# Optimization experiments

Hardware: AMD Instinct MI355X
Metric: run time of the kernel (lower is better)

Reference implementation:

```python
import jax, jax.numpy as jnp
import numpy as np
from jax import lax

N_QUBITS = 4
N_LAYERS = 1
K = 4       # kernel_size = n_qubits
S = 2       # stride
CDTYPE = jnp.complex64


def _rz(theta):
    # theta: (B,) or scalar -> (B,2,2) or (2,2) complex RZ matrix diag(e^{-i t/2}, e^{i t/2})
    p = jnp.exp(-0.5j * theta.astype(CDTYPE))
    q = jnp.exp(0.5j * theta.astype(CDTYPE))
    z = jnp.zeros_like(p)
    return jnp.stack([jnp.stack([p, z], -1), jnp.stack([z, q], -1)], -2)


def _ry(theta):
    c = jnp.cos(theta / 2).astype(CDTYPE)
    s = jnp.sin(theta / 2).astype(CDTYPE)
    return jnp.stack([jnp.stack([c, -s], -1), jnp.stack([s, c], -1)], -2)


def _apply_1q(state, U, wire):
    # state: (B,2,2,2,2); U: (B,2,2) per-sample or (2,2) shared
    s = jnp.moveaxis(state, 1 + wire, -1)
    if U.ndim == 3:
        s = jnp.einsum('bij,b...j->b...i', U, s)
    else:
        s = jnp.einsum('ij,b...j->b...i', U, s)
    return jnp.moveaxis(s, -1, 1 + wire)


def _apply_crz(state, theta, c, t):
    # CRZ is diagonal: diag(1,1,e^{-i t/2},e^{+i t/2}) in |control,target> basis
    one = jnp.ones((), CDTYPE)
    d = jnp.stack([jnp.stack([one, one]),
                   jnp.stack([jnp.exp(-0.5j * theta).astype(CDTYPE),
                              jnp.exp(0.5j * theta).astype(CDTYPE)])])  # (2,2)[ctrl,tgt]
    s = jnp.moveaxis(state, [1 + c, 1 + t], [-2, -1])
    return jnp.moveaxis(s * d, [-2, -1], [1 + c, 1 + t])


def _qcircuit(inputs, weights):
    # inputs: (B, 16) encoding angles; weights: (n_layers, 2*n_qubits)
    B, n_in = inputs.shape
    var_per_qubit = n_in // N_QUBITS + 1  # = 5 for 16 inputs
    # Hadamard on every qubit applied to |0000> gives the uniform state (amp = 1/4)
    state = jnp.full((B,) + (2,) * N_QUBITS, 0.25, dtype=CDTYPE)
    # data encoding: alternating RZ/RY per qubit
    for q in range(N_QUBITS):
        for i in range(var_per_qubit):
            idx = q * var_per_qubit + i
            if idx < n_in:
                theta = inputs[:, idx]
                U = _rz(theta) if i % 2 == 0 else _ry(theta)
                state = _apply_1q(state, U, q)
    # variational layer(s): ring of CRZ then RY on each wire
    for l in range(weights.shape[0]):
        for i in range(N_QUBITS):
            state = _apply_crz(state, weights[l, i], i, (i + 1) % N_QUBITS)
        for j in range(N_QUBITS):
            state = _apply_1q(state, _ry(weights[l, N_QUBITS + j]), j)
    # <Z_q> expectation values
    p = (state * jnp.conj(state)).real  # (B,2,2,2,2)
    evs = []
    for q in range(N_QUBITS):
        axes = tuple(a for a in range(1, 1 + N_QUBITS) if a != 1 + q)
        pq = jnp.sum(p, axis=axes)  # (B,2)
        evs.append(pq[:, 0] - pq[:, 1])
    return jnp.stack(evs, -1)  # (B, 4)


def reference(X, weights):
    # X: (B, 1, H, W)
    B = X.shape[0]
    # all sliding 4x4/stride-2 patches, feature order (c, kh, kw) matches torch.flatten
    patches = lax.conv_general_dilated_patches(X, (K, K), (S, S), 'VALID')  # (B,16,ox,oy)
    ox, oy = patches.shape[2], patches.shape[3]
    flat = jnp.transpose(patches, (0, 2, 3, 1)).reshape(B * ox * oy, -1)  # row-major patch order
    out = _qcircuit(flat, weights)  # (B*ox*oy, 4)
    # reproduce torch.cat(dim=1).view(bs, n_qubits, ox, oy) ordering exactly
    return out.reshape(B, ox * oy * N_QUBITS).reshape(B, N_QUBITS, ox, oy)


def setup_inputs() -> dict:
    key = jax.random.key(0)
    kx, kw = jax.random.split(key)
    X = jax.random.normal(kx, (128, 1, 192, 192), dtype=jnp.float32)
    weights = jax.random.normal(kw, (N_LAYERS, 2 * N_QUBITS), dtype=jnp.float32)
    return {"X": X, "weights": weights}
```

## Files before the change

### kernel.cpp

```cpp
#include <hip/hip_runtime.h>

namespace {

constexpr int IMG = 192;
constexpr int OX = 95, OY = 95;
constexpr int NPB = OX * OY;
constexpr int BATCH = 128;
constexpr int JP = 48;
constexpr int PERIMG = OX * JP;
constexpr int TOTAL = BATCH * PERIMG;
constexpr int NWG = TOTAL / 256;
constexpr int CHUNK = NWG / 8;

__device__ __forceinline__ float2 cmul(float2 a, float2 b) {
    return make_float2(a.x*b.x - a.y*b.y, a.x*b.y + a.y*b.x);
}

__device__ __forceinline__ void qubit_chain(
    float s0, float c0, float s1, float c1, float s2, float c2,
    float s3, float c3, float s4, float c4,
    float& m, float2& cq)
{
    float C0 = c0*c0 - s0*s0, S0 = 2.f*s0*c0;
    float C2 = c2*c2 - s2*s2, S2 = 2.f*s2*c2;
    float C4 = c4*c4 - s4*s4, S4f = 2.f*s4*c4;
    float2 u0 = make_float2(c1 - s1*C0, -s1*S0);
    float2 u1 = make_float2(s1 + c1*C0,  c1*S0);
    u1 = cmul(u1, make_float2(C2, S2));
    float2 n0 = make_float2(c3*u0.x - s3*u1.x, c3*u0.y - s3*u1.y);
    float2 n1 = make_float2(s3*u0.x + c3*u1.x, s3*u0.y + c3*u1.y);
    n1 = cmul(n1, make_float2(C4, S4f));
    m  = (n0.x*n0.x + n0.y*n0.y) - (n1.x*n1.x + n1.y*n1.y);
    cq = make_float2(n0.x*n1.x + n0.y*n1.y, n0.x*n1.y - n0.y*n1.x);
}

__device__ __forceinline__ float4 patch_ev(
    const float sh[4][6], const float ch[4][6], int o,
    const float cw[4], const float sw[4], const float ehx[4], const float ehy[4],
    const float Kq[4], const float S4v[4])
{
    float m[4]; float2 cq[4];
    qubit_chain(sh[0][o+0],ch[0][o+0], sh[0][o+1],ch[0][o+1], sh[0][o+2],ch[0][o+2],
                sh[0][o+3],ch[0][o+3], sh[1][o+0],ch[1][o+0], m[0], cq[0]);
    qubit_chain(sh[1][o+1],ch[1][o+1], sh[1][o+2],ch[1][o+2], sh[1][o+3],ch[1][o+3],
                sh[2][o+0],ch[2][o+0], sh[2][o+1],ch[2][o+1], m[1], cq[1]);
    qubit_chain(sh[2][o+2],ch[2][o+2], sh[2][o+3],ch[2][o+3], sh[3][o+0],ch[3][o+0],
                sh[3][o+1],ch[3][o+1], sh[3][o+2],ch[3][o+2], m[2], cq[2]);
    {
        float s = sh[3][o+3], c = ch[3][o+3];
        m[3]  = 0.f;
        cq[3] = make_float2(c*c - s*s, 2.f*s*c);
    }

    float ev[4];
#pragma unroll
    for (int q = 0; q < 4; ++q) {
        int jm = (q + 3) & 3, jp = (q + 1) & 3;
        float hmC = 0.5f * m[jm];
        float2 aC = make_float2((1.f + cw[jm]) + hmC * (1.f - cw[jm]),
                                sw[jm] * (1.f - hmC));
        float hmT = 0.5f * m[jp];
        float2 aT = make_float2((1.f + cw[q]) + hmT * (1.f - cw[q]),
                                sw[q] * (1.f - hmT));
        float2 t = cmul(aC, aT);
        t = cmul(t, make_float2(ehx[q], ehy[q]));
        ev[q] = Kq[q] * m[q] - S4v[q] * (cq[q].x * t.x - cq[q].y * t.y);
    }
    return make_float4(ev[0], ev[1], ev[2], ev[3]);
}

__global__ __launch_bounds__(256) void quanv_kernel(
    const float* __restrict__ X, const float* __restrict__ W,
    float* __restrict__ out)
{
    int orig = blockIdx.x;
    int wg = (orig & 7) * CHUNK + (orig >> 3);
    int tid = wg * 256 + threadIdx.x;
    int b  = tid / PERIMG;
    int r  = tid - b * PERIMG;
    int px = r / JP;
    int j  = r - px * JP;
    const bool hasB = (j < JP - 1);

    const float* img = X + (size_t)b * (IMG*IMG) + (2*px) * IMG + 4*j;
    const int c45 = hasB ? 4 : 0;

    float raw[4][6];
#pragma unroll
    for (int di = 0; di < 4; ++di) {
        const float* rp = img + di * IMG;
        float4 v  = *reinterpret_cast<const float4*>(rp);
        float2 w2 = *reinterpret_cast<const float2*>(rp + c45);
        raw[di][0] = v.x; raw[di][1] = v.y; raw[di][2] = v.z; raw[di][3] = v.w;
        raw[di][4] = w2.x; raw[di][5] = w2.y;
    }

    float cw[4], sw[4], ehx[4], ehy[4], Kq[4], S4v[4];
#pragma unroll
    for (int k = 0; k < 4; ++k) {
        float shh, chh, sry, cry;
        __sincosf(0.5f * W[k], &shh, &chh);
        __sincosf(W[4 + k], &sry, &cry);
        cw[k]  = chh*chh - shh*shh;
        sw[k]  = 2.f * chh * shh;
        ehx[k] = chh;
        ehy[k] = -shh;
        Kq[k]  = 0.5f  * cry;
        S4v[k] = 0.25f * sry;
    }

    float sh[4][6], ch[4][6];
#pragma unroll
    for (int di = 0; di < 4; ++di)
#pragma unroll
        for (int cc = 0; cc < 6; ++cc)
            __sincosf(0.5f * raw[di][cc], &sh[di][cc], &ch[di][cc]);

    float4 evA = patch_ev(sh, ch, 0, cw, sw, ehx, ehy, Kq, S4v);
    float4 evB = patch_ev(sh, ch, 2, cw, sw, ehx, ehy, Kq, S4v);

    float4* o4 = reinterpret_cast<float4*>(out) + (size_t)b * NPB + px * OY + 2*j;
    o4[0] = evA;
    if (hasB) o4[1] = evB;
}

}

extern "C" void kernel_launch(void* const* d_in, const int* in_sizes, int n_in,
                              void* d_out, int out_size, void* d_ws, size_t ws_size,
                              hipStream_t stream) {
    const float* X = (const float*)d_in[0];
    const float* W = (const float*)d_in[1];
    float* out = (float*)d_out;
    quanv_kernel<<<NWG, 256, 0, stream>>>(X, W, out);
}
```

Measured before the change: 16.80 us.

## Use Bloch-vector chain per qubit and precompute weight constants in a prologue kernel

Each qubit's encoding chain is rewritten as a Bloch-vector rotation on full-angle sincos values instead of half-angle complex amplitudes. The expectation combine is expanded algebraically into fused multiply-adds against constant coefficients. Those coefficients come from the weights and are now computed once by a tiny single-thread kernel into the workspace, rather than in every thread. The aim is fewer ALU operations per thread, at the cost of an extra kernel launch and a serial dependency between the two launches.

```diff
diff --git a/kernel.cpp b/kernel.cpp
--- a/kernel.cpp
+++ b/kernel.cpp
@@ -16,61 +16,98 @@
     return make_float2(a.x*b.x - a.y*b.y, a.x*b.y + a.y*b.x);
 }
 
-__device__ __forceinline__ void qubit_chain(
+__global__ void wconst_kernel(const float* __restrict__ W, float* __restrict__ ws)
+{
+    if (threadIdx.x != 0) return;
+    float cw[4], sw[4], ehx[4], ehy[4], S4[4];
+#pragma unroll
+    for (int k = 0; k < 4; ++k) {
+        float sh, ch, sry, cry;
+        __sincosf(0.5f * W[k], &sh, &ch);
+        __sincosf(W[4 + k], &sry, &cry);
+        cw[k] = ch*ch - sh*sh;  sw[k] = 2.f*ch*sh;
+        ehx[k] = ch;  ehy[k] = -sh;
+        S4[k] = 0.25f * sry;
+        ws[32 + k] = cry;
+    }
+#pragma unroll
+    for (int q = 0; q < 4; ++q) {
+        int qm = (q + 3) & 3;
+        float2 AC = make_float2(1.f + cw[qm],  sw[qm]);
+        float2 BC = make_float2(1.f - cw[qm], -sw[qm]);
+        float2 AT = make_float2(1.f + cw[q],   sw[q]);
+        float2 BT = make_float2(1.f - cw[q],  -sw[q]);
+        float2 G  = make_float2(S4[q]*ehx[q], S4[q]*ehy[q]);
+        float2 P = cmul(cmul(G, AC), AT);
+        float2 Q = cmul(cmul(G, BC), AT);
+        float2 R = cmul(cmul(G, AC), BT);
+        float2 S = cmul(cmul(G, BC), BT);
+        ws[q*8+0] = P.x; ws[q*8+1] = P.y;
+        ws[q*8+2] = Q.x; ws[q*8+3] = Q.y;
+        ws[q*8+4] = R.x; ws[q*8+5] = R.y;
+        ws[q*8+6] = S.x; ws[q*8+7] = S.y;
+    }
+}
+
+__device__ __forceinline__ void bloch_chain(
     float s0, float c0, float s1, float c1, float s2, float c2,
     float s3, float c3, float s4, float c4,
-    float& m, float2& cq)
+    float& z, float& cx, float& cy)
 {
-    float C0 = c0*c0 - s0*s0, S0 = 2.f*s0*c0;
-    float C2 = c2*c2 - s2*s2, S2 = 2.f*s2*c2;
-    float C4 = c4*c4 - s4*s4, S4f = 2.f*s4*c4;
-    float2 u0 = make_float2(c1 - s1*C0, -s1*S0);
-    float2 u1 = make_float2(s1 + c1*C0,  c1*S0);
-    u1 = cmul(u1, make_float2(C2, S2));
-    float2 n0 = make_float2(c3*u0.x - s3*u1.x, c3*u0.y - s3*u1.y);
-    float2 n1 = make_float2(s3*u0.x + c3*u1.x, s3*u0.y + c3*u1.y);
-    n1 = cmul(n1, make_float2(C4, S4f));
-    m  = (n0.x*n0.x + n0.y*n0.y) - (n1.x*n1.x + n1.y*n1.y);
-    cq = make_float2(n0.x*n1.x + n0.y*n1.y, n0.x*n1.y - n0.y*n1.x);
+    float x1  = c0 * c1;
+    float z1n = c0 * s1;
+    float x2 = x1*c2 - s0*s2;
+    float y2 = x1*s2 + s0*c2;
+    float x3 = x2*c3 - z1n*s3;
+    float z3 = -z1n*c3 - x2*s3;
+    cx = x3*c4 - y2*s4;
+    cy = x3*s4 + y2*c4;
+    z  = z3;
 }
 
 __device__ __forceinline__ float4 patch_ev(
-    const float sh[4][6], const float ch[4][6], int o,
-    const float cw[4], const float sw[4], const float ehx[4], const float ehy[4],
-    const float Kq[4], const float S4v[4])
+    const float sn[4][6], const float cs[4][6], int o,
+    const float* __restrict__ wsc)
 {
-    float m[4]; float2 cq[4];
-    qubit_chain(sh[0][o+0],ch[0][o+0], sh[0][o+1],ch[0][o+1], sh[0][o+2],ch[0][o+2],
-                sh[0][o+3],ch[0][o+3], sh[1][o+0],ch[1][o+0], m[0], cq[0]);
-    qubit_chain(sh[1][o+1],ch[1][o+1], sh[1][o+2],ch[1][o+2], sh[1][o+3],ch[1][o+3],
-                sh[2][o+0],ch[2][o+0], sh[2][o+1],ch[2][o+1], m[1], cq[1]);
-    qubit_chain(sh[2][o+2],ch[2][o+2], sh[2][o+3],ch[2][o+3], sh[3][o+0],ch[3][o+0],
-                sh[3][o+1],ch[3][o+1], sh[3][o+2],ch[3][o+2], m[2], cq[2]);
+    float z[3], cqx[4], cqy[4];
+    bloch_chain(sn[0][o+0],cs[0][o+0], sn[0][o+1],cs[0][o+1], sn[0][o+2],cs[0][o+2],
+                sn[0][o+3],cs[0][o+3], sn[1][o+0],cs[1][o+0], z[0], cqx[0], cqy[0]);
+    bloch_chain(sn[1][o+1],cs[1][o+1], sn[1][o+2],cs[1][o+2], sn[1][o+3],cs[1][o+3],
+                sn[2][o+0],cs[2][o+0], sn[2][o+1],cs[2][o+1], z[1], cqx[1], cqy[1]);
+    bloch_chain(sn[2][o+2],cs[2][o+2], sn[2][o+3],cs[2][o+3], sn[3][o+0],cs[3][o+0],
+                sn[3][o+1],cs[3][o+1], sn[3][o+2],cs[3][o+2], z[2], cqx[2], cqy[2]);
+    cqx[3] = cs[3][o+3];  cqy[3] = sn[3][o+3];
+
+    float zz = z[0] * z[2];
+    float ev[4];
     {
-        float s = sh[3][o+3], c = ch[3][o+3];
-        m[3]  = 0.f;
-        cq[3] = make_float2(c*c - s*s, 2.f*s*c);
+        float Tx = fmaf(z[1], wsc[4], wsc[0]);
+        float Ty = fmaf(z[1], wsc[5], wsc[1]);
+        float t = cqx[0]*Tx - cqy[0]*Ty;
+        ev[0] = fmaf(wsc[32], z[0], -t);
     }
-
-    float ev[4];
-#pragma unroll
-    for (int q = 0; q < 4; ++q) {
-        int jm = (q + 3) & 3, jp = (q + 1) & 3;
-        float hmC = 0.5f * m[jm];
-        float2 aC = make_float2((1.f + cw[jm]) + hmC * (1.f - cw[jm]),
-                                sw[jm] * (1.f - hmC));
-        float hmT = 0.5f * m[jp];
-        float2 aT = make_float2((1.f + cw[q]) + hmT * (1.f - cw[q]),
-                                sw[q] * (1.f - hmT));
-        float2 t = cmul(aC, aT);
-        t = cmul(t, make_float2(ehx[q], ehy[q]));
-        ev[q] = Kq[q] * m[q] - S4v[q] * (cq[q].x * t.x - cq[q].y * t.y);
+    {
+        float Tx = fmaf(zz, wsc[8+6], fmaf(z[2], wsc[8+4], fmaf(z[0], wsc[8+2], wsc[8+0])));
+        float Ty = fmaf(zz, wsc[8+7], fmaf(z[2], wsc[8+5], fmaf(z[0], wsc[8+3], wsc[8+1])));
+        float t = cqx[1]*Tx - cqy[1]*Ty;
+        ev[1] = fmaf(wsc[33], z[1], -t);
+    }
+    {
+        float Tx = fmaf(z[1], wsc[16+2], wsc[16+0]);
+        float Ty = fmaf(z[1], wsc[16+3], wsc[16+1]);
+        float t = cqx[2]*Tx - cqy[2]*Ty;
+        ev[2] = fmaf(wsc[34], z[2], -t);
+    }
+    {
+        float Tx = fmaf(zz, wsc[24+6], fmaf(z[0], wsc[24+4], fmaf(z[2], wsc[24+2], wsc[24+0])));
+        float Ty = fmaf(zz, wsc[24+7], fmaf(z[0], wsc[24+5], fmaf(z[2], wsc[24+3], wsc[24+1])));
+        ev[3] = fmaf(-cqx[3], Tx, cqy[3]*Ty);
     }
     return make_float4(ev[0], ev[1], ev[2], ev[3]);
 }
 
 __global__ __launch_bounds__(256) void quanv_kernel(
-    const float* __restrict__ X, const float* __restrict__ W,
+    const float* __restrict__ X, const float* __restrict__ wsc,
     float* __restrict__ out)
 {
     int orig = blockIdx.x;
@@ -95,29 +132,15 @@
         raw[di][4] = w2.x; raw[di][5] = w2.y;
     }
 
-    float cw[4], sw[4], ehx[4], ehy[4], Kq[4], S4v[4];
-#pragma unroll
-    for (int k = 0; k < 4; ++k) {
-        float shh, chh, sry, cry;
-        __sincosf(0.5f * W[k], &shh, &chh);
-        __sincosf(W[4 + k], &sry, &cry);
-        cw[k]  = chh*chh - shh*shh;
-        sw[k]  = 2.f * chh * shh;
-        ehx[k] = chh;
-        ehy[k] = -shh;
-        Kq[k]  = 0.5f  * cry;
-        S4v[k] = 0.25f * sry;
-    }
-
-    float sh[4][6], ch[4][6];
+    float sn[4][6], cs[4][6];
 #pragma unroll
     for (int di = 0; di < 4; ++di)
 #pragma unroll
         for (int cc = 0; cc < 6; ++cc)
-            __sincosf(0.5f * raw[di][cc], &sh[di][cc], &ch[di][cc]);
+            __sincosf(raw[di][cc], &sn[di][cc], &cs[di][cc]);
 
-    float4 evA = patch_ev(sh, ch, 0, cw, sw, ehx, ehy, Kq, S4v);
-    float4 evB = patch_ev(sh, ch, 2, cw, sw, ehx, ehy, Kq, S4v);
+    float4 evA = patch_ev(sn, cs, 0, wsc);
+    float4 evB = patch_ev(sn, cs, 2, wsc);
 
     float4* o4 = reinterpret_cast<float4*>(out) + (size_t)b * NPB + px * OY + 2*j;
     o4[0] = evA;
@@ -132,5 +155,7 @@
     const float* X = (const float*)d_in[0];
     const float* W = (const float*)d_in[1];
     float* out = (float*)d_out;
-    quanv_kernel<<<NWG, 256, 0, stream>>>(X, W, out);
+    float* ws  = (float*)d_ws;
+    wconst_kernel<<<1, 64, 0, stream>>>(W, ws);
+    quanv_kernel<<<NWG, 256, 0, stream>>>(X, ws, out);
 }
```

Measured after the change: 18.34 us. 9.2% more time.
